# Kernel tuning notes

Measured on AMD Instinct MI355X. Metric: run time of the kernel, lower is better.

Reference implementation:

```python
import jax, jax.numpy as jnp
from jax import lax
import numpy as np

BINS = 25
K = 5  # entropy patch size
EPS = 1e-5


def conv2d(x, w, b, stride, pad):
    y = lax.conv_general_dilated(x, w, (stride, stride), [(pad, pad), (pad, pad)],
                                 dimension_numbers=("NCHW", "OIHW", "NCHW"))
    return y + b[None, :, None, None]


def group_norm_per_channel(x, w, b):
    # GroupNorm with num_groups == num_channels: per-channel norm over H,W (biased var)
    mu = x.mean(axis=(2, 3), keepdims=True)
    v = x.var(axis=(2, 3), keepdims=True)
    return (x - mu) / jnp.sqrt(v + EPS) * w[None, :, None, None] + b[None, :, None, None]


def channel_entropy(x):
    # x: (b,c,h,w). Unfold into 5x5 patches, per-patch histc(bins=25) over patch
    # values using that patch's min/max range (torch.histc default), then entropy.
    b, c, h, w = x.shape
    ho, wo = h - K + 1, w - K + 1
    # (b,c,K*K,L) -- fixed 25-position loop, vectorized over all data dims
    patches = jnp.stack([x[:, :, i:i + ho, j:j + wo]
                         for i in range(K) for j in range(K)], axis=2)
    patches = patches.reshape(b, c, K * K, ho * wo)
    mn = patches.min(axis=2, keepdims=True)
    mx = patches.max(axis=2, keepdims=True)
    rng = jnp.where(mx > mn, mx - mn, jnp.ones_like(mx))
    bins = jnp.clip(jnp.floor((patches - mn) / rng * BINS), 0, BINS - 1).astype(jnp.int32)
    # histogram via comparison one-hot: (b,c,L,BINS)
    counts = (bins[..., None] == jnp.arange(BINS, dtype=jnp.int32)).sum(axis=2)
    pk = counts.astype(x.dtype) / (K * K)
    ent = (-pk * jnp.log(jnp.clip(pk, 1e-5, 1.0 - 1e-5))).sum(axis=-1).mean(axis=-1)  # (b,c)
    return ent[:, :, None, None]


def instance_norm_ent(x, w, b):
    ent = channel_entropy(lax.stop_gradient(x))
    mu = x.mean(axis=(2, 3), keepdims=True)
    n = x.shape[2] * x.shape[3]
    v = x.var(axis=(2, 3), keepdims=True) * (n / (n - 1))  # unbiased var (torch default)
    return (x - mu) / jnp.sqrt(v + EPS) * w[None, :, None, None] * ent + b[None, :, None, None]


def setup_inputs() -> dict:
    key = jax.random.key(0)
    ks = jax.random.split(key, 24)
    s = 0.05
    d = {
        "x": jax.random.normal(ks[0], (64, 3, 224, 224), jnp.float32),
        "conv0_w": jax.random.normal(ks[1], (8, 3, 7, 7), jnp.float32) * s,
        "conv0_b": jax.random.normal(ks[2], (8,), jnp.float32) * s,
        "conv1_w": jax.random.normal(ks[3], (16, 8, 5, 5), jnp.float32) * s,
        "conv1_b": jax.random.normal(ks[4], (16,), jnp.float32) * s,
        "conv2_w": jax.random.normal(ks[5], (32, 16, 3, 3), jnp.float32) * s,
        "conv2_b": jax.random.normal(ks[6], (32,), jnp.float32) * s,
        "gn0_w": jnp.ones((8,), jnp.float32) + jax.random.normal(ks[7], (8,), jnp.float32) * s,
        "gn0_b": jax.random.normal(ks[8], (8,), jnp.float32) * s,
        "n1_w": jnp.ones((16,), jnp.float32) + jax.random.normal(ks[9], (16,), jnp.float32) * s,
        "n1_b": jax.random.normal(ks[10], (16,), jnp.float32) * s,
        "n2_w": jnp.ones((32,), jnp.float32) + jax.random.normal(ks[11], (32,), jnp.float32) * s,
        "n2_b": jax.random.normal(ks[12], (32,), jnp.float32) * s,
        "bn_g": jnp.ones((10368,), jnp.float32) + jax.random.normal(ks[13], (10368,), jnp.float32) * s,
        "bn_b": jax.random.normal(ks[14], (10368,), jnp.float32) * s,
        "fc1_w": jax.random.normal(ks[15], (32, 10368), jnp.float32) * 0.01,
        "fc1_b": jax.random.normal(ks[16], (32,), jnp.float32) * s,
        "shape_w": jax.random.normal(ks[17], (5, 32), jnp.float32) * s,
        "shape_b": jax.random.normal(ks[18], (5,), jnp.float32) * s,
        "vern_w": jax.random.normal(ks[19], (2, 32), jnp.float32) * s,
        "vern_b": jax.random.normal(ks[20], (2,), jnp.float32) * s,
    }
    return d


def reference(x, conv0_w, conv0_b, conv1_w, conv1_b, conv2_w, conv2_b,
              gn0_w, gn0_b, n1_w, n1_b, n2_w, n2_b,
              bn_g, bn_b, fc1_w, fc1_b, shape_w, shape_b, vern_w, vern_b):
    h = conv2d(x, conv0_w, conv0_b, 4, 2)          # (b,8,56,56)
    h = jax.nn.relu(group_norm_per_channel(h, gn0_w, gn0_b))
    h = conv2d(h, conv1_w, conv1_b, 3, 1)          # (b,16,18,18)
    h = jax.nn.relu(instance_norm_ent(h, n1_w, n1_b))
    h = conv2d(h, conv2_w, conv2_b, 1, 1)          # (b,32,18,18)
    h = jax.nn.relu(instance_norm_ent(h, n2_w, n2_b))
    h = h.reshape(h.shape[0], -1)                  # (b,10368)
    # BatchNorm1d (training mode: batch stats, biased var)
    mu = h.mean(axis=0)
    v = h.var(axis=0)
    h = (h - mu) / jnp.sqrt(v + EPS) * bn_g + bn_b
    h = jax.nn.relu(h @ fc1_w.T + fc1_b)           # (b,32)
    out_shape = jax.nn.softmax(h @ shape_w.T + shape_b, axis=-1)
    out_vern = jax.nn.softmax(h @ vern_w.T + vern_b, axis=-1)
    return (out_shape, out_vern)
```

## Files before the change

### kernel.cpp

```cpp
#include <hip/hip_runtime.h>
#include <math.h>

#define EPSD 1e-5


__device__ __forceinline__ double waveReduceSumD(double v) {
#pragma unroll
    for (int off = 32; off > 0; off >>= 1)
        v += __shfl_down(v, off, 64);
    return v;
}

template <int NW>
__device__ __forceinline__ double blockReduceSumD(double v, double* buf) {
    int lane = threadIdx.x & 63;
    int w = threadIdx.x >> 6;
    v = waveReduceSumD(v);
    __syncthreads();
    if (lane == 0) buf[w] = v;
    __syncthreads();
    double tot = 0.0;
#pragma unroll
    for (int i = 0; i < NW; i++) tot += buf[i];
    return tot;
}

__device__ __forceinline__ void build_ent_tab(float* tab) {
    int t = threadIdx.x;
    if (t < 26) {
        if (t == 0) tab[0] = 0.f;
        else {
            double pk = (double)t / 25.0;
            double cl = fmin(fmax(pk, 1e-5), 1.0 - 1e-5);
            tab[t] = (float)(-pk * log(cl));
        }
    }
}

__device__ __forceinline__ float patch_ent(const float* ch, int py, int px, const float* tab) {
    float pv[25];
#pragma unroll
    for (int i = 0; i < 5; i++)
#pragma unroll
        for (int j = 0; j < 5; j++)
            pv[i * 5 + j] = ch[(py + i) * 18 + px + j];
    float mn = pv[0], mx = pv[0];
#pragma unroll
    for (int k = 1; k < 25; k++) { mn = fminf(mn, pv[k]); mx = fmaxf(mx, pv[k]); }
    float rng = (mx > mn) ? (mx - mn) : 1.0f;
    unsigned long long a0 = 0ull, a1 = 0ull;
    int a2 = 0;
#pragma unroll
    for (int k = 0; k < 25; k++) {
        float tt = (pv[k] - mn) / rng * 25.0f;
        int bi = (int)floorf(tt);
        bi = bi < 0 ? 0 : (bi > 24 ? 24 : bi);
        unsigned sh0 = ((unsigned)(5 * bi)) & 63u;
        unsigned sh1 = ((unsigned)(5 * bi - 60)) & 63u;
        a0 += (bi < 12) ? (1ull << sh0) : 0ull;
        a1 += (bi >= 12 && bi < 24) ? (1ull << sh1) : 0ull;
        a2 += (bi == 24) ? 1 : 0;
    }
    float ent = 0.f;
#pragma unroll
    for (int k = 0; k < 12; k++) ent += tab[(a0 >> (5 * k)) & 31ull];
#pragma unroll
    for (int k = 0; k < 12; k++) ent += tab[(a1 >> (5 * k)) & 31ull];
    ent += tab[a2];
    return ent;
}

__global__ __launch_bounds__(256, 6) void k_conv0(const float* __restrict__ x,
                                                  const float* __restrict__ w,
                                                  const float* __restrict__ bias,
                                                  float* __restrict__ h0raw,
                                                  double* __restrict__ part0) {
    __shared__ __align__(16) float tile[4332];
    __shared__ double redbuf[4][16];
    int tl = blockIdx.x;
    int b = blockIdx.y;
    int t = threadIdx.x;
    for (int i = t; i < 4332; i += 256) tile[i] = 0.f;
    int y_base = tl * 16 - 2;
    const float* xb = x + (size_t)b * 150528;
    float acc[8];
#pragma unroll
    for (int c = 0; c < 8; c++) acc[c] = bias[c];
    int ry = t / 56, ox = t % 56;
    for (int ci = 0; ci < 3; ci++) {
        __syncthreads();
        for (int i = t; i < 1064; i += 256) {
            int r = i / 56, f4 = i % 56;
            int yIn = y_base + r;
            if (yIn >= 0 && yIn < 224) {
                float4 v = *(const float4*)&xb[ci * 50176 + yIn * 224 + f4 * 4];
                float* tp = tile + r * 228;
                tp[114 + f4] = v.x;
                tp[171 + f4] = v.y;
                tp[f4 + 1]   = v.z;
                tp[58 + f4]  = v.w;
            }
        }
        __syncthreads();
        if (t < 224) {
            const float* wci = w + ci * 49;
#pragma unroll
            for (int ky = 0; ky < 7; ky++) {
                const float* rp = tile + (4 * ry + ky) * 228;
#pragma unroll
                for (int kx = 0; kx < 7; kx++) {
                    float v = rp[(kx & 3) * 57 + ox + (kx >> 2)];
#pragma unroll
                    for (int c = 0; c < 8; c++)
                        acc[c] += v * wci[c * 147 + ky * 7 + kx];
                }
            }
        }
    }
    if (t < 224) {
        int oy = tl * 4 + ry;
        int opix = oy * 56 + ox;
#pragma unroll
        for (int c = 0; c < 8; c++)
            h0raw[((size_t)b * 8 + c) * 3136 + opix] = acc[c];
    } else {
#pragma unroll
        for (int c = 0; c < 8; c++) acc[c] = 0.f;
    }
    int wv = t >> 6, lane = t & 63;
#pragma unroll
    for (int c = 0; c < 8; c++) {
        double rs = waveReduceSumD((double)acc[c]);
        double rq = waveReduceSumD((double)acc[c] * (double)acc[c]);
        if (lane == 0) { redbuf[wv][c * 2] = rs; redbuf[wv][c * 2 + 1] = rq; }
    }
    __syncthreads();
    if (t < 16) {
        double tot = redbuf[0][t] + redbuf[1][t] + redbuf[2][t] + redbuf[3][t];
        part0[(((size_t)b * 14 + tl) << 4) + t] = tot;
    }
}

__global__ __launch_bounds__(1024) void k_conv1_ent(const float* __restrict__ h0raw,
                                                    const double* __restrict__ part0,
                                                    const float* __restrict__ gw,
                                                    const float* __restrict__ gb,
                                                    const float* __restrict__ w,
                                                    const float* __restrict__ bias,
                                                    const float* __restrict__ nw,
                                                    const float* __restrict__ nb,
                                                    float* __restrict__ h1) {
    __shared__ __align__(16) float xin2[25088];
    __shared__ float vals[1296];
    __shared__ float tab[26];
    __shared__ float gnp[16];
    __shared__ double redbuf[16][2];
    __shared__ double entbuf[16];
    __shared__ float prm[4][3];
    int b = blockIdx.x >> 2;
    int grp = blockIdx.x & 3;
    int t = threadIdx.x;
    if (t < 8) {
        double s = 0.0, s2 = 0.0;
        const double* p = part0 + ((size_t)b * 14) * 16;
        for (int tile = 0; tile < 14; tile++) {
            s += p[tile * 16 + t * 2];
            s2 += p[tile * 16 + t * 2 + 1];
        }
        double mean = s / 3136.0;
        double var = s2 / 3136.0 - mean * mean;
        double rstd = 1.0 / sqrt(var + EPSD);
        double sc = (double)gw[t] * rstd;
        gnp[t] = (float)sc;
        gnp[8 + t] = (float)((double)gb[t] - mean * sc);
    }
    build_ent_tab(tab);
    __syncthreads();
    for (int i = t; i < 25088; i += 1024) {
        int ci = i / 3136, px = i - ci * 3136;
        float v = fmaxf(h0raw[(size_t)b * 25088 + i] * gnp[ci] + gnp[8 + ci], 0.f);
        xin2[(ci >> 1) * 6272 + px * 2 + (ci & 1)] = v;
    }
    __syncthreads();

    int wv = t >> 6, lane = t & 63;
    int c = wv >> 2;
    int q = wv & 3;
    int j_u = __builtin_amdgcn_readfirstlane(grp * 4 + c);
    const float* wg = w + (size_t)j_u * 200;
    float* vch = vals + c * 324;
    float bv = bias[j_u];
    double s = 0.0, s2 = 0.0;
    for (int p = q * 81 + lane; p < q * 81 + 81; p += 64) {
        int oy = p / 18, ox = p - oy * 18;
        int y0 = oy * 3 - 1, x0 = ox * 3 - 1;
        float acc = bv;
        if (oy >= 1 && ox >= 1) {
#pragma unroll
            for (int c2 = 0; c2 < 4; c2++) {
                const float* xp = xin2 + c2 * 6272 + (y0 * 56 + x0) * 2;
                const float* wp0 = wg + (2 * c2) * 25;
#pragma unroll
                for (int ky = 0; ky < 5; ky++)
#pragma unroll
                    for (int kx = 0; kx < 5; kx++) {
                        float2 v = *(const float2*)&xp[(ky * 56 + kx) * 2];
                        acc += v.x * wp0[ky * 5 + kx];
                        acc += v.y * wp0[25 + ky * 5 + kx];
                    }
            }
        } else {
            int ky0 = y0 < 0 ? 1 : 0;
            int kx0 = x0 < 0 ? 1 : 0;
            for (int c2 = 0; c2 < 4; c2++) {
                const float* xp = xin2 + c2 * 6272;
                const float* wp0 = wg + (2 * c2) * 25;
                for (int ky = ky0; ky < 5; ky++) {
                    for (int kx = kx0; kx < 5; kx++) {
                        float2 v = *(const float2*)&xp[((y0 + ky) * 56 + x0 + kx) * 2];
                        acc += v.x * wp0[ky * 5 + kx];
                        acc += v.y * wp0[25 + ky * 5 + kx];
                    }
                }
            }
        }
        vch[p] = acc;
        s += (double)acc; s2 += (double)acc * (double)acc;
    }
    s = waveReduceSumD(s);
    s2 = waveReduceSumD(s2);
    if (lane == 0) { redbuf[wv][0] = s; redbuf[wv][1] = s2; }
    __syncthreads();
    double ent = 0.0;
    if (lane < 49) {
        int pi = q * 49 + lane;
        ent = (double)patch_ent(vch, pi / 14, pi % 14, tab);
    }
    ent = waveReduceSumD(ent);
    if (lane == 0) entbuf[wv] = ent;
    __syncthreads();
    if (t < 4) {
        double ss = 0.0, qq = 0.0, ee = 0.0;
        for (int k = 0; k < 4; k++) {
            ss += redbuf[t * 4 + k][0];
            qq += redbuf[t * 4 + k][1];
            ee += entbuf[t * 4 + k];
        }
        double entmean = ee / 196.0;
        double mean = ss / 324.0;
        double varb = qq / 324.0 - mean * mean;
        double varu = varb * (324.0 / 323.0);
        double rstd = 1.0 / sqrt(varu + EPSD);
        prm[t][0] = (float)mean;
        prm[t][1] = (float)((double)nw[grp * 4 + t] * entmean * rstd);
        prm[t][2] = nb[grp * 4 + t];
    }
    __syncthreads();
    float* outp = h1 + ((size_t)b * 16 + grp * 4) * 324;
    for (int i = t; i < 1296; i += 1024) {
        int cc = i / 324;
        outp[i] = fmaxf((vals[i] - prm[cc][0]) * prm[cc][1] + prm[cc][2], 0.f);
    }
}

__global__ __launch_bounds__(256) void k_conv2_ent(const float* __restrict__ in,
                                                   const float* __restrict__ w,
                                                   const float* __restrict__ bias,
                                                   const float* __restrict__ nw,
                                                   const float* __restrict__ nb,
                                                   float* __restrict__ out) {
    __shared__ __align__(16) float xin2[5184];
    __shared__ float vals[324];
    __shared__ float tab[26];
    __shared__ double rbuf[4];
    int b = blockIdx.x >> 5;
    int c = blockIdx.x & 31;
    int t = threadIdx.x;
    const float* xb = in + (size_t)b * 5184;
    for (int i = t; i < 5184; i += 256) {
        int ci = i / 324, px = i - ci * 324;
        xin2[(ci >> 1) * 648 + px * 2 + (ci & 1)] = xb[i];
    }
    build_ent_tab(tab);
    __syncthreads();
    const float* wc = w + c * 144;
    float bv = bias[c];
    double s = 0.0, s2 = 0.0;
    {
        int oy = 1 + (t >> 4), ox = 1 + (t & 15);
        int base = ((oy - 1) * 18 + (ox - 1)) * 2;
        float acc = bv;
#pragma unroll
        for (int c2 = 0; c2 < 8; c2++) {
            const float* xp = xin2 + c2 * 648 + base;
            const float* wp = wc + c2 * 18;
#pragma unroll
            for (int ky = 0; ky < 3; ky++)
#pragma unroll
                for (int kx = 0; kx < 3; kx++) {
                    float2 v = *(const float2*)&xp[(ky * 18 + kx) * 2];
                    acc += v.x * wp[ky * 3 + kx];
                    acc += v.y * wp[9 + ky * 3 + kx];
                }
        }
        vals[oy * 18 + ox] = acc;
        s += (double)acc; s2 += (double)acc * (double)acc;
    }
    if (t < 68) {
        int oy, ox;
        if (t < 18)      { oy = 0;      ox = t; }
        else if (t < 36) { oy = 17;     ox = t - 18; }
        else if (t < 52) { oy = t - 35; ox = 0; }
        else             { oy = t - 51; ox = 17; }
        int y0 = oy - 1, x0 = ox - 1;
        int ky0 = y0 < 0 ? 1 : 0;
        int ky1 = (18 - y0) < 3 ? 2 : 3;
        int kx0 = x0 < 0 ? 1 : 0;
        int kx1 = (18 - x0) < 3 ? 2 : 3;
        float acc = bv;
        for (int c2 = 0; c2 < 8; c2++) {
            const float* xp = xin2 + c2 * 648;
            const float* wp = wc + c2 * 18;
            for (int ky = ky0; ky < ky1; ky++) {
                for (int kx = kx0; kx < kx1; kx++) {
                    float2 v = *(const float2*)&xp[((y0 + ky) * 18 + x0 + kx) * 2];
                    acc += v.x * wp[ky * 3 + kx];
                    acc += v.y * wp[9 + ky * 3 + kx];
                }
            }
        }
        vals[oy * 18 + ox] = acc;
        s += (double)acc; s2 += (double)acc * (double)acc;
    }
    __syncthreads();
    double ent = 0.0;
    if (t < 196) ent = (double)patch_ent(vals, t / 14, t % 14, tab);
    double entmean = blockReduceSumD<4>(ent, rbuf) / 196.0;
    double ssum  = blockReduceSumD<4>(s, rbuf);
    double s2sum = blockReduceSumD<4>(s2, rbuf);
    double mean = ssum / 324.0;
    double varb = s2sum / 324.0 - mean * mean;
    double varu = varb * (324.0 / 323.0);
    double rstd = 1.0 / sqrt(varu + EPSD);
    float sc = (float)((double)nw[c] * entmean * rstd);
    float mu = (float)mean;
    float be = nb[c];
    float* outp = out + ((size_t)b * 32 + c) * 324;
    for (int idx = t; idx < 324; idx += 256)
        outp[idx] = fmaxf((vals[idx] - mu) * sc + be, 0.f);
}

__global__ __launch_bounds__(256) void k_bnstats(const float* __restrict__ h2,
                                                 const float* __restrict__ g,
                                                 const float* __restrict__ bb,
                                                 float* __restrict__ scale,
                                                 float* __restrict__ shift) {
    __shared__ double sb[4][64], qb[4][64];
    int lane = threadIdx.x & 63;
    int q = threadIdx.x >> 6;
    int f = blockIdx.x * 64 + lane;
    double s = 0.0, s2 = 0.0;
    for (int b = q * 16; b < q * 16 + 16; b++) {
        double v = (double)h2[(size_t)b * 10368 + f];
        s += v; s2 += v * v;
    }
    sb[q][lane] = s; qb[q][lane] = s2;
    __syncthreads();
    if (threadIdx.x < 64) {
        double S = sb[0][lane] + sb[1][lane] + sb[2][lane] + sb[3][lane];
        double Q = qb[0][lane] + qb[1][lane] + qb[2][lane] + qb[3][lane];
        double mean = S / 64.0;
        double var = Q / 64.0 - mean * mean;
        double rstd = 1.0 / sqrt(var + EPSD);
        double sc = (double)g[f] * rstd;
        scale[f] = (float)sc;
        shift[f] = (float)((double)bb[f] - mean * sc);
    }
}

__global__ __launch_bounds__(256) void k_fc1(const float* __restrict__ h2,
                                             const float* __restrict__ scale,
                                             const float* __restrict__ shift,
                                             const float* __restrict__ w1,
                                             const float* __restrict__ b1,
                                             float* __restrict__ fcout) {
    __shared__ double rbuf[4];
    int b = blockIdx.x >> 5;
    int j = blockIdx.x & 31;
    const float* hb = h2 + (size_t)b * 10368;
    const float* wj = w1 + (size_t)j * 10368;
    double acc = 0.0;
    for (int f = threadIdx.x * 4; f < 10368; f += 1024) {
        float4 h4 = *(const float4*)&hb[f];
        float4 s4 = *(const float4*)&scale[f];
        float4 t4 = *(const float4*)&shift[f];
        float4 w4 = *(const float4*)&wj[f];
        acc += (double)((h4.x * s4.x + t4.x) * w4.x);
        acc += (double)((h4.y * s4.y + t4.y) * w4.y);
        acc += (double)((h4.z * s4.z + t4.z) * w4.z);
        acc += (double)((h4.w * s4.w + t4.w) * w4.w);
    }
    acc = blockReduceSumD<4>(acc, rbuf);
    if (threadIdx.x == 0)
        fcout[b * 32 + j] = (float)fmax(acc + (double)b1[j], 0.0);
}

__global__ __launch_bounds__(64) void k_heads(const float* __restrict__ fc,
                                              const float* __restrict__ sw,
                                              const float* __restrict__ sb,
                                              const float* __restrict__ vw,
                                              const float* __restrict__ vb,
                                              float* __restrict__ out) {
    int b = threadIdx.x;
    double h[32];
#pragma unroll
    for (int i = 0; i < 32; i++) h[i] = (double)fc[b * 32 + i];
    double lg[5];
    double mx = -1e300;
#pragma unroll
    for (int k = 0; k < 5; k++) {
        double a = (double)sb[k];
#pragma unroll
        for (int i = 0; i < 32; i++) a += h[i] * (double)sw[k * 32 + i];
        lg[k] = a;
        mx = fmax(mx, a);
    }
    double se = 0.0;
#pragma unroll
    for (int k = 0; k < 5; k++) { lg[k] = exp(lg[k] - mx); se += lg[k]; }
#pragma unroll
    for (int k = 0; k < 5; k++) out[b * 5 + k] = (float)(lg[k] / se);
    double l0 = (double)vb[0], l1 = (double)vb[1];
#pragma unroll
    for (int i = 0; i < 32; i++) { l0 += h[i] * (double)vw[i]; l1 += h[i] * (double)vw[32 + i]; }
    double m = fmax(l0, l1);
    double e0 = exp(l0 - m), e1 = exp(l1 - m);
    double inv = 1.0 / (e0 + e1);
    out[320 + b * 2 + 0] = (float)(e0 * inv);
    out[320 + b * 2 + 1] = (float)(e1 * inv);
}

extern "C" void kernel_launch(void* const* d_in, const int* in_sizes, int n_in,
                              void* d_out, int out_size, void* d_ws, size_t ws_size,
                              hipStream_t stream) {
    const float* x       = (const float*)d_in[0];
    const float* conv0_w = (const float*)d_in[1];
    const float* conv0_b = (const float*)d_in[2];
    const float* conv1_w = (const float*)d_in[3];
    const float* conv1_b = (const float*)d_in[4];
    const float* conv2_w = (const float*)d_in[5];
    const float* conv2_b = (const float*)d_in[6];
    const float* gn0_w   = (const float*)d_in[7];
    const float* gn0_b   = (const float*)d_in[8];
    const float* n1_w    = (const float*)d_in[9];
    const float* n1_b    = (const float*)d_in[10];
    const float* n2_w    = (const float*)d_in[11];
    const float* n2_b    = (const float*)d_in[12];
    const float* bn_g    = (const float*)d_in[13];
    const float* bn_b    = (const float*)d_in[14];
    const float* fc1_w   = (const float*)d_in[15];
    const float* fc1_b   = (const float*)d_in[16];
    const float* shape_w = (const float*)d_in[17];
    const float* shape_b = (const float*)d_in[18];
    const float* vern_w  = (const float*)d_in[19];
    const float* vern_b  = (const float*)d_in[20];
    float* out = (float*)d_out;

    double* part0 = (double*)d_ws;
    float* fbase   = (float*)(part0 + 14336);
    float* h0raw   = fbase;
    float* h1      = h0raw + 1605632;
    float* h2      = h1 + 331776;
    float* bnscale = h2 + 663552;
    float* bnshift = bnscale + 10368;
    float* fc      = bnshift + 10368;

    k_conv0<<<dim3(14, 64), dim3(256), 0, stream>>>(x, conv0_w, conv0_b, h0raw, part0);
    k_conv1_ent<<<dim3(256), dim3(1024), 0, stream>>>(h0raw, part0, gn0_w, gn0_b,
                                                      conv1_w, conv1_b, n1_w, n1_b, h1);
    k_conv2_ent<<<dim3(2048), dim3(256), 0, stream>>>(h1, conv2_w, conv2_b, n2_w, n2_b, h2);
    k_bnstats<<<dim3(162), dim3(256), 0, stream>>>(h2, bn_g, bn_b, bnscale, bnshift);
    k_fc1<<<dim3(2048), dim3(256), 0, stream>>>(h2, bnscale, bnshift, fc1_w, fc1_b, fc);
    k_heads<<<dim3(1), dim3(64), 0, stream>>>(fc, shape_w, shape_b, vern_w, vern_b, out);
}
```

Before: 227.3 us.

## Compute multiple output channels per thread in conv1/conv2 entropy kernels

Restructures conv1 and conv2 so each thread computes 8 or 16 output channels for one pixel, reusing each loaded input value across channels instead of reloading it per channel. Blocks now cover half the channels of a sample, which cuts redundant input staging: conv2 goes from 32 blocks per sample to 2, and conv1 from 4 to 2. Per-channel stats and entropy are then computed per wave over the shared vals buffer. The trade-off is far fewer blocks (128 each), so parallelism drops, some threads sit idle during the conv phase (only 324 of 512 active), and register pressure rises.

```diff
diff --git a/kernel.cpp b/kernel.cpp
--- a/kernel.cpp
+++ b/kernel.cpp
@@ -141,24 +141,24 @@
     }
 }
 
-__global__ __launch_bounds__(1024) void k_conv1_ent(const float* __restrict__ h0raw,
-                                                    const double* __restrict__ part0,
-                                                    const float* __restrict__ gw,
-                                                    const float* __restrict__ gb,
-                                                    const float* __restrict__ w,
-                                                    const float* __restrict__ bias,
-                                                    const float* __restrict__ nw,
-                                                    const float* __restrict__ nb,
-                                                    float* __restrict__ h1) {
+__global__ __launch_bounds__(512) void k_conv1_ent(const float* __restrict__ h0raw,
+                                                   const double* __restrict__ part0,
+                                                   const float* __restrict__ gw,
+                                                   const float* __restrict__ gb,
+                                                   const float* __restrict__ w,
+                                                   const float* __restrict__ bias,
+                                                   const float* __restrict__ nw,
+                                                   const float* __restrict__ nb,
+                                                   float* __restrict__ h1) {
     __shared__ __align__(16) float xin2[25088];
-    __shared__ float vals[1296];
+    __shared__ float vals[2592];
     __shared__ float tab[26];
     __shared__ float gnp[16];
-    __shared__ double redbuf[16][2];
-    __shared__ double entbuf[16];
-    __shared__ float prm[4][3];
-    int b = blockIdx.x >> 2;
-    int grp = blockIdx.x & 3;
+    __shared__ double redbuf[8][2];
+    __shared__ double entbuf[8];
+    __shared__ float prm[8][3];
+    int b = blockIdx.x >> 1;
+    int half = blockIdx.x & 1;
     int t = threadIdx.x;
     if (t < 8) {
         double s = 0.0, s2 = 0.0;
@@ -176,37 +176,35 @@
     }
     build_ent_tab(tab);
     __syncthreads();
-    for (int i = t; i < 25088; i += 1024) {
+    for (int i = t; i < 25088; i += 512) {
         int ci = i / 3136, px = i - ci * 3136;
         float v = fmaxf(h0raw[(size_t)b * 25088 + i] * gnp[ci] + gnp[8 + ci], 0.f);
         xin2[(ci >> 1) * 6272 + px * 2 + (ci & 1)] = v;
     }
     __syncthreads();
 
-    int wv = t >> 6, lane = t & 63;
-    int c = wv >> 2;
-    int q = wv & 3;
-    int j_u = __builtin_amdgcn_readfirstlane(grp * 4 + c);
-    const float* wg = w + (size_t)j_u * 200;
-    float* vch = vals + c * 324;
-    float bv = bias[j_u];
-    double s = 0.0, s2 = 0.0;
-    for (int p = q * 81 + lane; p < q * 81 + 81; p += 64) {
-        int oy = p / 18, ox = p - oy * 18;
+    const float* wbase = w + (size_t)(half * 8) * 200;
+    if (t < 324) {
+        int oy = t / 18, ox = t - oy * 18;
         int y0 = oy * 3 - 1, x0 = ox * 3 - 1;
-        float acc = bv;
+        float acc[8];
+#pragma unroll
+        for (int c = 0; c < 8; c++) acc[c] = bias[half * 8 + c];
         if (oy >= 1 && ox >= 1) {
 #pragma unroll
             for (int c2 = 0; c2 < 4; c2++) {
                 const float* xp = xin2 + c2 * 6272 + (y0 * 56 + x0) * 2;
-                const float* wp0 = wg + (2 * c2) * 25;
 #pragma unroll
                 for (int ky = 0; ky < 5; ky++)
 #pragma unroll
                     for (int kx = 0; kx < 5; kx++) {
                         float2 v = *(const float2*)&xp[(ky * 56 + kx) * 2];
-                        acc += v.x * wp0[ky * 5 + kx];
-                        acc += v.y * wp0[25 + ky * 5 + kx];
+#pragma unroll
+                        for (int c = 0; c < 8; c++) {
+                            const float* wp0 = wbase + c * 200 + (2 * c2) * 25;
+                            acc[c] += v.x * wp0[ky * 5 + kx];
+                            acc[c] += v.y * wp0[25 + ky * 5 + kx];
+                        }
                     }
             }
         } else {
@@ -214,140 +212,165 @@
             int kx0 = x0 < 0 ? 1 : 0;
             for (int c2 = 0; c2 < 4; c2++) {
                 const float* xp = xin2 + c2 * 6272;
-                const float* wp0 = wg + (2 * c2) * 25;
                 for (int ky = ky0; ky < 5; ky++) {
                     for (int kx = kx0; kx < 5; kx++) {
                         float2 v = *(const float2*)&xp[((y0 + ky) * 56 + x0 + kx) * 2];
-                        acc += v.x * wp0[ky * 5 + kx];
-                        acc += v.y * wp0[25 + ky * 5 + kx];
+#pragma unroll
+                        for (int c = 0; c < 8; c++) {
+                            const float* wp0 = wbase + c * 200 + (2 * c2) * 25;
+                            acc[c] += v.x * wp0[ky * 5 + kx];
+                            acc[c] += v.y * wp0[25 + ky * 5 + kx];
+                        }
                     }
                 }
             }
         }
-        vch[p] = acc;
-        s += (double)acc; s2 += (double)acc * (double)acc;
-    }
-    s = waveReduceSumD(s);
-    s2 = waveReduceSumD(s2);
-    if (lane == 0) { redbuf[wv][0] = s; redbuf[wv][1] = s2; }
-    __syncthreads();
-    double ent = 0.0;
-    if (lane < 49) {
-        int pi = q * 49 + lane;
-        ent = (double)patch_ent(vch, pi / 14, pi % 14, tab);
-    }
-    ent = waveReduceSumD(ent);
-    if (lane == 0) entbuf[wv] = ent;
-    __syncthreads();
-    if (t < 4) {
-        double ss = 0.0, qq = 0.0, ee = 0.0;
-        for (int k = 0; k < 4; k++) {
-            ss += redbuf[t * 4 + k][0];
-            qq += redbuf[t * 4 + k][1];
-            ee += entbuf[t * 4 + k];
-        }
-        double entmean = ee / 196.0;
-        double mean = ss / 324.0;
-        double varb = qq / 324.0 - mean * mean;
+#pragma unroll
+        for (int c = 0; c < 8; c++) vals[c * 324 + t] = acc[c];
+    }
+    __syncthreads();
+
+    int wv = t >> 6, lane = t & 63;
+    {
+        const float* vch = vals + wv * 324;
+        double s = 0.0, s2 = 0.0;
+        for (int i = lane; i < 324; i += 64) {
+            double v = (double)vch[i];
+            s += v; s2 += v * v;
+        }
+        s = waveReduceSumD(s);
+        s2 = waveReduceSumD(s2);
+        double ent = 0.0;
+        for (int pi = lane; pi < 196; pi += 64)
+            ent += (double)patch_ent(vch, pi / 14, pi % 14, tab);
+        ent = waveReduceSumD(ent);
+        if (lane == 0) { redbuf[wv][0] = s; redbuf[wv][1] = s2; entbuf[wv] = ent; }
+    }
+    __syncthreads();
+    if (t < 8) {
+        double entmean = entbuf[t] / 196.0;
+        double mean = redbuf[t][0] / 324.0;
+        double varb = redbuf[t][1] / 324.0 - mean * mean;
         double varu = varb * (324.0 / 323.0);
         double rstd = 1.0 / sqrt(varu + EPSD);
         prm[t][0] = (float)mean;
-        prm[t][1] = (float)((double)nw[grp * 4 + t] * entmean * rstd);
-        prm[t][2] = nb[grp * 4 + t];
-    }
-    __syncthreads();
-    float* outp = h1 + ((size_t)b * 16 + grp * 4) * 324;
-    for (int i = t; i < 1296; i += 1024) {
+        prm[t][1] = (float)((double)nw[half * 8 + t] * entmean * rstd);
+        prm[t][2] = nb[half * 8 + t];
+    }
+    __syncthreads();
+    float* outp = h1 + ((size_t)b * 16 + half * 8) * 324;
+    for (int i = t; i < 2592; i += 512) {
         int cc = i / 324;
         outp[i] = fmaxf((vals[i] - prm[cc][0]) * prm[cc][1] + prm[cc][2], 0.f);
     }
 }
 
-__global__ __launch_bounds__(256) void k_conv2_ent(const float* __restrict__ in,
+__global__ __launch_bounds__(512) void k_conv2_ent(const float* __restrict__ in,
                                                    const float* __restrict__ w,
                                                    const float* __restrict__ bias,
                                                    const float* __restrict__ nw,
                                                    const float* __restrict__ nb,
                                                    float* __restrict__ out) {
     __shared__ __align__(16) float xin2[5184];
-    __shared__ float vals[324];
+    __shared__ float vals[5184];
     __shared__ float tab[26];
-    __shared__ double rbuf[4];
-    int b = blockIdx.x >> 5;
-    int c = blockIdx.x & 31;
+    __shared__ double redbuf[16][2];
+    __shared__ double entbuf[16];
+    __shared__ float prm[16][3];
+    int b = blockIdx.x >> 1;
+    int half = blockIdx.x & 1;
     int t = threadIdx.x;
     const float* xb = in + (size_t)b * 5184;
-    for (int i = t; i < 5184; i += 256) {
+    for (int i = t; i < 5184; i += 512) {
         int ci = i / 324, px = i - ci * 324;
         xin2[(ci >> 1) * 648 + px * 2 + (ci & 1)] = xb[i];
     }
     build_ent_tab(tab);
     __syncthreads();
-    const float* wc = w + c * 144;
-    float bv = bias[c];
-    double s = 0.0, s2 = 0.0;
-    {
-        int oy = 1 + (t >> 4), ox = 1 + (t & 15);
-        int base = ((oy - 1) * 18 + (ox - 1)) * 2;
-        float acc = bv;
-#pragma unroll
-        for (int c2 = 0; c2 < 8; c2++) {
-            const float* xp = xin2 + c2 * 648 + base;
-            const float* wp = wc + c2 * 18;
-#pragma unroll
-            for (int ky = 0; ky < 3; ky++)
-#pragma unroll
-                for (int kx = 0; kx < 3; kx++) {
-                    float2 v = *(const float2*)&xp[(ky * 18 + kx) * 2];
-                    acc += v.x * wp[ky * 3 + kx];
-                    acc += v.y * wp[9 + ky * 3 + kx];
-                }
-        }
-        vals[oy * 18 + ox] = acc;
-        s += (double)acc; s2 += (double)acc * (double)acc;
-    }
-    if (t < 68) {
-        int oy, ox;
-        if (t < 18)      { oy = 0;      ox = t; }
-        else if (t < 36) { oy = 17;     ox = t - 18; }
-        else if (t < 52) { oy = t - 35; ox = 0; }
-        else             { oy = t - 51; ox = 17; }
+    const float* wbase = w + (size_t)(half * 16) * 144;
+    if (t < 324) {
+        int oy = t / 18, ox = t - oy * 18;
         int y0 = oy - 1, x0 = ox - 1;
-        int ky0 = y0 < 0 ? 1 : 0;
-        int ky1 = (18 - y0) < 3 ? 2 : 3;
-        int kx0 = x0 < 0 ? 1 : 0;
-        int kx1 = (18 - x0) < 3 ? 2 : 3;
-        float acc = bv;
-        for (int c2 = 0; c2 < 8; c2++) {
-            const float* xp = xin2 + c2 * 648;
-            const float* wp = wc + c2 * 18;
-            for (int ky = ky0; ky < ky1; ky++) {
-                for (int kx = kx0; kx < kx1; kx++) {
-                    float2 v = *(const float2*)&xp[((y0 + ky) * 18 + x0 + kx) * 2];
-                    acc += v.x * wp[ky * 3 + kx];
-                    acc += v.y * wp[9 + ky * 3 + kx];
+        float acc[16];
+#pragma unroll
+        for (int c = 0; c < 16; c++) acc[c] = bias[half * 16 + c];
+        if (oy >= 1 && oy <= 16 && ox >= 1 && ox <= 16) {
+#pragma unroll
+            for (int c2 = 0; c2 < 8; c2++) {
+                const float* xp = xin2 + c2 * 648 + (y0 * 18 + x0) * 2;
+#pragma unroll
+                for (int ky = 0; ky < 3; ky++)
+#pragma unroll
+                    for (int kx = 0; kx < 3; kx++) {
+                        float2 v = *(const float2*)&xp[(ky * 18 + kx) * 2];
+#pragma unroll
+                        for (int c = 0; c < 16; c++) {
+                            const float* wp = wbase + c * 144 + c2 * 18;
+                            acc[c] += v.x * wp[ky * 3 + kx];
+                            acc[c] += v.y * wp[9 + ky * 3 + kx];
+                        }
+                    }
+            }
+        } else {
+            int ky0 = y0 < 0 ? 1 : 0;
+            int ky1 = (18 - y0) < 3 ? 2 : 3;
+            int kx0 = x0 < 0 ? 1 : 0;
+            int kx1 = (18 - x0) < 3 ? 2 : 3;
+            for (int c2 = 0; c2 < 8; c2++) {
+                const float* xp = xin2 + c2 * 648;
+                for (int ky = ky0; ky < ky1; ky++) {
+                    for (int kx = kx0; kx < kx1; kx++) {
+                        float2 v = *(const float2*)&xp[((y0 + ky) * 18 + x0 + kx) * 2];
+#pragma unroll
+                        for (int c = 0; c < 16; c++) {
+                            const float* wp = wbase + c * 144 + c2 * 18;
+                            acc[c] += v.x * wp[ky * 3 + kx];
+                            acc[c] += v.y * wp[9 + ky * 3 + kx];
+                        }
+                    }
                 }
             }
         }
-        vals[oy * 18 + ox] = acc;
-        s += (double)acc; s2 += (double)acc * (double)acc;
-    }
-    __syncthreads();
-    double ent = 0.0;
-    if (t < 196) ent = (double)patch_ent(vals, t / 14, t % 14, tab);
-    double entmean = blockReduceSumD<4>(ent, rbuf) / 196.0;
-    double ssum  = blockReduceSumD<4>(s, rbuf);
-    double s2sum = blockReduceSumD<4>(s2, rbuf);
-    double mean = ssum / 324.0;
-    double varb = s2sum / 324.0 - mean * mean;
-    double varu = varb * (324.0 / 323.0);
-    double rstd = 1.0 / sqrt(varu + EPSD);
-    float sc = (float)((double)nw[c] * entmean * rstd);
-    float mu = (float)mean;
-    float be = nb[c];
-    float* outp = out + ((size_t)b * 32 + c) * 324;
-    for (int idx = t; idx < 324; idx += 256)
-        outp[idx] = fmaxf((vals[idx] - mu) * sc + be, 0.f);
+#pragma unroll
+        for (int c = 0; c < 16; c++) vals[c * 324 + t] = acc[c];
+    }
+    __syncthreads();
+
+    int wv = t >> 6, lane = t & 63;
+#pragma unroll
+    for (int k = 0; k < 2; k++) {
+        int cc = wv * 2 + k;
+        const float* vch = vals + cc * 324;
+        double s = 0.0, s2 = 0.0;
+        for (int i = lane; i < 324; i += 64) {
+            double v = (double)vch[i];
+            s += v; s2 += v * v;
+        }
+        s = waveReduceSumD(s);
+        s2 = waveReduceSumD(s2);
+        double ent = 0.0;
+        for (int pi = lane; pi < 196; pi += 64)
+            ent += (double)patch_ent(vch, pi / 14, pi % 14, tab);
+        ent = waveReduceSumD(ent);
+        if (lane == 0) { redbuf[cc][0] = s; redbuf[cc][1] = s2; entbuf[cc] = ent; }
+    }
+    __syncthreads();
+    if (t < 16) {
+        double entmean = entbuf[t] / 196.0;
+        double mean = redbuf[t][0] / 324.0;
+        double varb = redbuf[t][1] / 324.0 - mean * mean;
+        double varu = varb * (324.0 / 323.0);
+        double rstd = 1.0 / sqrt(varu + EPSD);
+        prm[t][0] = (float)mean;
+        prm[t][1] = (float)((double)nw[half * 16 + t] * entmean * rstd);
+        prm[t][2] = nb[half * 16 + t];
+    }
+    __syncthreads();
+    float* outp = out + ((size_t)b * 32 + half * 16) * 324;
+    for (int i = t; i < 5184; i += 512) {
+        int cc = i / 324;
+        outp[i] = fmaxf((vals[i] - prm[cc][0]) * prm[cc][1] + prm[cc][2], 0.f);
+    }
 }
 
 __global__ __launch_bounds__(256) void k_bnstats(const float* __restrict__ h2,
@@ -476,9 +499,9 @@
     float* fc      = bnshift + 10368;
 
     k_conv0<<<dim3(14, 64), dim3(256), 0, stream>>>(x, conv0_w, conv0_b, h0raw, part0);
-    k_conv1_ent<<<dim3(256), dim3(1024), 0, stream>>>(h0raw, part0, gn0_w, gn0_b,
-                                                      conv1_w, conv1_b, n1_w, n1_b, h1);
-    k_conv2_ent<<<dim3(2048), dim3(256), 0, stream>>>(h1, conv2_w, conv2_b, n2_w, n2_b, h2);
+    k_conv1_ent<<<dim3(128), dim3(512), 0, stream>>>(h0raw, part0, gn0_w, gn0_b,
+                                                     conv1_w, conv1_b, n1_w, n1_b, h1);
+    k_conv2_ent<<<dim3(128), dim3(512), 0, stream>>>(h1, conv2_w, conv2_b, n2_w, n2_b, h2);
     k_bnstats<<<dim3(162), dim3(256), 0, stream>>>(h2, bn_g, bn_b, bnscale, bnshift);
     k_fc1<<<dim3(2048), dim3(256), 0, stream>>>(h2, bnscale, bnshift, fc1_w, fc1_b, fc);
     k_heads<<<dim3(1), dim3(64), 0, stream>>>(fc, shape_w, shape_b, vern_w, vern_b, out);
```

After: 289.8 us. 1.28x slower.
